# Performance work log

Measured on AMD Instinct MI355X. Metric: run time of the kernel, lower is better.

## Reference

```python
import jax, jax.numpy as jnp
import numpy as np

B, N, PATCH_DIM, HIDDEN, POS_SIZE = 16, 4096, 768, 768, 10240


def setup_inputs() -> dict:
    key = jax.random.key(0)
    k1, k2, k3, k4, k5 = jax.random.split(key, 5)
    pixel_values = jax.random.uniform(k1, (B, N, PATCH_DIM), dtype=jnp.float32)
    pixel_position_ids = jax.random.randint(k2, (B, N, 2), 0, POS_SIZE, dtype=jnp.int32)
    padding_mask = jax.random.randint(k3, (B, N), 0, 2).astype(bool)
    W_proj = jax.random.normal(k4, (HIDDEN, PATCH_DIM), dtype=jnp.float32) * 0.02
    pos_table = jax.random.normal(k5, (2, POS_SIZE, HIDDEN), dtype=jnp.float32) * 0.02
    return {
        "pixel_values": pixel_values,
        "pixel_position_ids": pixel_position_ids,
        "padding_mask": padding_mask,
        "W_proj": W_proj,
        "pos_table": pos_table,
    }


def reference(pixel_values, pixel_position_ids, padding_mask, W_proj, pos_table):
    # Rescale pixels to [-1, 1]
    x = 2.0 * (pixel_values - 0.5)
    # Linear(patch_dim -> hidden), bias=False: h = x @ W^T  -> [B, N, H]
    h = jnp.einsum("bnp,hp->bnh", x, W_proj)
    # Position embedding lookup. Original uses one_hot @ table; mathematically
    # identical to a direct gather per axis followed by a sum over the 2 axes.
    pos = jnp.clip(pixel_position_ids, 0, None)  # [B, N, 2]
    pe = pos_table[0][pos[..., 0]] + pos_table[1][pos[..., 1]]  # [B, N, H]
    pe = jnp.where(padding_mask[..., None], 0.0, pe)
    h = h + pe
    # masked_fill padded positions with 0
    h = jnp.where(padding_mask[..., None], 0.0, h)
    return h
```

## Files before the change

kernel.cpp:

```cpp
#include <hip/hip_runtime.h>
#include <hip/hip_bf16.h>

typedef __bf16 bf16_t;
typedef bf16_t bf16x4 __attribute__((ext_vector_type(4)));
typedef bf16_t bf16x8 __attribute__((ext_vector_type(8)));
typedef float f32x4 __attribute__((ext_vector_type(4)));

constexpr int NB   = 16;
constexpr int NN   = 4096;
constexpr int PD   = 768;
constexpr int HID  = 768;
constexpr int PSZ  = 10240;
constexpr int MT   = NB * NN;
constexpr int BM   = 128;
constexpr int BN   = 128;
constexpr int BK   = 32;
constexpr int NT   = PD / BK;
constexpr int LDSC = 132;
constexpr size_t PVN = (size_t)MT * PD;
constexpr size_t WN  = (size_t)HID * PD;

__device__ __forceinline__ bf16x8 cvt8_affine(const float4& x, const float4& y,
                                              float s, float o) {
    bf16x8 r;
    r[0] = (bf16_t)__builtin_fmaf(s, x.x, o);
    r[1] = (bf16_t)__builtin_fmaf(s, x.y, o);
    r[2] = (bf16_t)__builtin_fmaf(s, x.z, o);
    r[3] = (bf16_t)__builtin_fmaf(s, x.w, o);
    r[4] = (bf16_t)__builtin_fmaf(s, y.x, o);
    r[5] = (bf16_t)__builtin_fmaf(s, y.y, o);
    r[6] = (bf16_t)__builtin_fmaf(s, y.z, o);
    r[7] = (bf16_t)__builtin_fmaf(s, y.w, o);
    return r;
}

__device__ __forceinline__ bf16x4 cvt4_affine(const float4& x, float s, float o) {
    bf16x4 r;
    r[0] = (bf16_t)__builtin_fmaf(s, x.x, o);
    r[1] = (bf16_t)__builtin_fmaf(s, x.y, o);
    r[2] = (bf16_t)__builtin_fmaf(s, x.z, o);
    r[3] = (bf16_t)__builtin_fmaf(s, x.w, o);
    return r;
}

__global__ __launch_bounds__(256)
void compact_cvt(const float* __restrict__ pv,
                 const int* __restrict__ mask,
                 const float* __restrict__ W,
                 bf16_t* __restrict__ Ab,
                 bf16_t* __restrict__ Wb,
                 int* __restrict__ rowmap,
                 int* __restrict__ counter,
                 float* __restrict__ out)
{
    const int bid = blockIdx.x;
    const int tid = threadIdx.x;
    if (bid < 1024) {
        __shared__ int ls_slot[64];
        const int rowbase = bid * 64;
        const int lane = tid & 63;
        const int wv   = tid >> 6;
        if (wv == 0) {
            const int mk = mask[rowbase + lane];
            const unsigned long long b = __ballot(mk == 0);
            const int total = __popcll(b);
            const int pos = __popcll(b & ((1ull << lane) - 1ull));
            int gb = 0;
            if (lane == 0) gb = atomicAdd(counter, total);
            gb = __shfl(gb, 0);
            const int slot = (mk == 0) ? (gb + pos) : -1;
            ls_slot[lane] = slot;
            if (slot >= 0) rowmap[slot] = rowbase + lane;
        }
        __syncthreads();
        for (int i = wv; i < 64; i += 4) {
            const int slot = ls_slot[i];
            const int grow = rowbase + i;
            if (slot >= 0) {
                const float* src = pv + (size_t)grow * PD + lane * 12;
                bf16_t* dst = Ab + (size_t)slot * PD + lane * 12;
                #pragma unroll
                for (int q = 0; q < 3; ++q) {
                    const float4 v = *(const float4*)(src + q * 4);
                    *(bf16x4*)(dst + q * 4) = cvt4_affine(v, 2.f, -1.f);
                }
            } else {
                float* dst = out + (size_t)grow * HID + lane * 12;
                const float4 z{0.f, 0.f, 0.f, 0.f};
                #pragma unroll
                for (int q = 0; q < 3; ++q)
                    *(float4*)(dst + q * 4) = z;
            }
        }
    } else {
        const size_t nu = WN / 8;
        for (size_t u = (size_t)(bid - 1024) * 256 + tid; u < nu;
             u += (size_t)64 * 256) {
            const float4 x = ((const float4*)W)[2 * u];
            const float4 y = ((const float4*)W)[2 * u + 1];
            *(bf16x8*)(Wb + 8 * u) = cvt8_affine(x, y, 1.f, 0.f);
        }
    }
}

__global__ __launch_bounds__(256)
void cvt_kernel(const float* __restrict__ pv, const float* __restrict__ W,
                bf16_t* __restrict__ Ab, bf16_t* __restrict__ Wb)
{
    const size_t nunits = (PVN + WN) / 8;
    const size_t stride = (size_t)gridDim.x * blockDim.x;
    for (size_t u = (size_t)blockIdx.x * blockDim.x + threadIdx.x;
         u < nunits; u += stride) {
        if (u < PVN / 8) {
            const float4 x = ((const float4*)pv)[2 * u];
            const float4 y = ((const float4*)pv)[2 * u + 1];
            *(bf16x8*)(Ab + 8 * u) = cvt8_affine(x, y, 2.f, -1.f);
        } else {
            const size_t v = u - PVN / 8;
            const float4 x = ((const float4*)W)[2 * v];
            const float4 y = ((const float4*)W)[2 * v + 1];
            *(bf16x8*)(Wb + 8 * v) = cvt8_affine(x, y, 1.f, 0.f);
        }
    }
}

__device__ __forceinline__ void gload16(const void* g, void* l) {
    __builtin_amdgcn_global_load_lds(
        (const __attribute__((address_space(1))) void*)g,
        (__attribute__((address_space(3))) void*)l, 16, 0, 0);
}

template <bool USE_MAP>
__global__ __launch_bounds__(256, 4)
void gemm_kernel(const bf16_t* __restrict__ Ab,
                 const bf16_t* __restrict__ Wb,
                 const int* __restrict__ posids,
                 const int* __restrict__ mask,
                 const float* __restrict__ ptab,
                 float* __restrict__ out,
                 const int* __restrict__ rowmap,
                 const int* __restrict__ counter)
{
    __shared__ alignas(16) unsigned char smem[32 * LDSC * 4];
    bf16_t* const Bsb = (bf16_t*)smem;
    float*  const Cs  = (float*)smem;

    int Mc = MT;
    int mt, nt;
    const int bid = blockIdx.x;
    if constexpr (USE_MAP) {
        Mc = counter[0];
        const int Mtiles = (Mc + BM - 1) / BM;
        const int nact = Mtiles * 6;
        if (bid >= nact) return;
        const int q = nact >> 3, rm = nact & 7;
        const int x = bid & 7, i = bid >> 3;
        const int logical = (x < rm ? x * (q + 1) : rm * (q + 1) + (x - rm) * q) + i;
        mt = logical / 6;
        nt = logical - mt * 6;
    } else {
        const int nwg = gridDim.x;
        const int cpx = nwg >> 3;
        const int logical = (bid & 7) * cpx + (bid >> 3);
        mt = logical / 6;
        nt = logical - mt * 6;
    }
    const int row0 = mt * BM;
    const int col0 = nt * BN;

    const int tid  = threadIdx.x;
    const int lane = tid & 63;
    const int wid  = tid >> 6;
    const int wm   = wid >> 1;
    const int wn   = wid & 1;

    const int srow = tid >> 2;
    const int sk   = (tid & 3) * 8;
    const bf16_t* b0 = Wb + (size_t)(col0 + srow) * PD + sk;
    const int lds_lo = srow * BK + sk;
    const int lds_hi = (srow + 64) * BK + sk;

    f32x4 acc[4][4];
    #pragma unroll
    for (int i = 0; i < 4; ++i)
        #pragma unroll
        for (int j = 0; j < 4; ++j)
            acc[i][j] = f32x4{0.f, 0.f, 0.f, 0.f};

    const int lr = lane & 15;
    const int kg = lane >> 4;
    const int b_rd_off = (wn * 64 + lr) * BK + kg * 8;

    const bf16_t* aF[4];
    #pragma unroll
    for (int i = 0; i < 4; ++i)
        aF[i] = Ab + (size_t)(row0 + wm * 64 + i * 16 + lr) * PD + kg * 8;

    gload16(b0,           Bsb + lds_lo);
    gload16(b0 + 64 * PD, Bsb + lds_hi);
    __syncthreads();

    int cur = 0;
    for (int t = 0; t < NT; ++t) {
        bf16x8 af[4];
        #pragma unroll
        for (int i = 0; i < 4; ++i)
            af[i] = *(const bf16x8*)(aF[i] + t * BK);

        if (t + 1 < NT) {
            const int k1 = (t + 1) * BK;
            const int nb = cur ^ 1;
            gload16(b0 + k1,           Bsb + nb * (BN * BK) + lds_lo);
            gload16(b0 + 64 * PD + k1, Bsb + nb * (BN * BK) + lds_hi);
        }

        bf16x8 bfv[4];
        #pragma unroll
        for (int i = 0; i < 4; ++i)
            bfv[i] = *(const bf16x8*)(Bsb + cur * (BN * BK) + b_rd_off + i * 16 * BK);

        #pragma unroll
        for (int i = 0; i < 4; ++i)
            #pragma unroll
            for (int j = 0; j < 4; ++j)
                acc[i][j] = __builtin_amdgcn_mfma_f32_16x16x32_bf16(
                    af[i], bfv[j], acc[i][j], 0, 0, 0);

        __syncthreads();
        cur ^= 1;
    }

    const int lrow_w  = wm * 16 + kg * 4;
    const int lcol_w  = wn * 64 + lr;
    const int rr = tid >> 3;
    const int cg = tid & 7;
    const int erow_local = (rr & 15) + (rr >> 4) * 64;

    int grow4[4], p04[4], p14[4];
    #pragma unroll
    for (int mi = 0; mi < 4; ++mi) {
        int crow = row0 + mi * 16 + erow_local;
        if constexpr (USE_MAP) {
            const int cc = crow < Mc ? crow : Mc - 1;
            grow4[mi] = rowmap[cc];
        } else {
            grow4[mi] = crow;
        }
        int p0 = posids[2 * grow4[mi]];
        int p1 = posids[2 * grow4[mi] + 1];
        p04[mi] = p0 < 0 ? 0 : p0;
        p14[mi] = p1 < 0 ? 0 : p1;
    }

    #pragma unroll
    for (int mi = 0; mi < 4; ++mi) {
        __syncthreads();
        #pragma unroll
        for (int r = 0; r < 4; ++r)
            #pragma unroll
            for (int ni = 0; ni < 4; ++ni)
                Cs[(lrow_w + r) * LDSC + lcol_w + ni * 16] = acc[mi][ni][r];
        __syncthreads();

        const int crow = row0 + mi * 16 + erow_local;
        if constexpr (USE_MAP) {
            if (crow >= Mc) continue;
            const float* t0 = ptab + (size_t)p04[mi] * HID + col0;
            const float* t1 = ptab + (size_t)PSZ * HID + (size_t)p14[mi] * HID + col0;
            float* orow = out + (size_t)grow4[mi] * HID + col0;
            #pragma unroll
            for (int j = 0; j < 4; ++j) {
                const int c = (cg + 8 * j) * 4;
                float4 v  = *(const float4*)&Cs[rr * LDSC + c];
                const float4 e0 = *(const float4*)(t0 + c);
                const float4 e1 = *(const float4*)(t1 + c);
                v.x += e0.x + e1.x;
                v.y += e0.y + e1.y;
                v.z += e0.z + e1.z;
                v.w += e0.w + e1.w;
                *(float4*)(orow + c) = v;
            }
        } else {
            const int grow = crow;
            float* orow = out + (size_t)grow * HID + col0;
            const int mk = mask[grow];
            if (mk) {
                const float4 z{0.f, 0.f, 0.f, 0.f};
                #pragma unroll
                for (int j = 0; j < 4; ++j)
                    *(float4*)(orow + (cg + 8 * j) * 4) = z;
            } else {
                const float* t0 = ptab + (size_t)p04[mi] * HID + col0;
                const float* t1 = ptab + (size_t)PSZ * HID + (size_t)p14[mi] * HID + col0;
                #pragma unroll
                for (int j = 0; j < 4; ++j) {
                    const int c = (cg + 8 * j) * 4;
                    float4 v  = *(const float4*)&Cs[rr * LDSC + c];
                    const float4 e0 = *(const float4*)(t0 + c);
                    const float4 e1 = *(const float4*)(t1 + c);
                    v.x += e0.x + e1.x;
                    v.y += e0.y + e1.y;
                    v.z += e0.z + e1.z;
                    v.w += e0.w + e1.w;
                    *(float4*)(orow + c) = v;
                }
            }
        }
    }
}

constexpr int LDSS = 40;

__global__ __launch_bounds__(256, 2)
void vpe_kernel(const float* __restrict__ pv,
                const int* __restrict__ posids,
                const int* __restrict__ mask,
                const float* __restrict__ W,
                const float* __restrict__ ptab,
                float* __restrict__ out)
{
    __shared__ alignas(16) bf16_t As[2][BM * LDSS];
    __shared__ alignas(16) bf16_t Bs[2][BM * LDSS];

    const int nwg = gridDim.x;
    const int cpx = nwg >> 3;
    const int logical = (blockIdx.x & 7) * cpx + (blockIdx.x >> 3);
    const int mt = logical / 6;
    const int nt = logical - mt * 6;
    const int row0 = mt * BM;
    const int col0 = nt * BN;

    const int tid  = threadIdx.x;
    const int lane = tid & 63;
    const int wid  = tid >> 6;
    const int wm   = wid >> 1;
    const int wn   = wid & 1;
    const int srow = tid >> 1;
    const int scol = (tid & 1) << 4;

    const float* aptr = pv + (size_t)(row0 + srow) * PD + scol;
    const float* bptr = W  + (size_t)(col0 + srow) * PD + scol;
    const int lds_w_off = srow * LDSS + scol;

    f32x4 acc[4][4];
    #pragma unroll
    for (int i = 0; i < 4; ++i)
        #pragma unroll
        for (int j = 0; j < 4; ++j)
            acc[i][j] = f32x4{0.f, 0.f, 0.f, 0.f};

    const int lr = lane & 15;
    const int kg = lane >> 4;
    const int a_rd_off = (wm * 64 + lr) * LDSS + kg * 8;
    const int b_rd_off = (wn * 64 + lr) * LDSS + kg * 8;

    float4 ra[4], rb[4];
    #pragma unroll
    for (int q = 0; q < 4; ++q) {
        ra[q] = *(const float4*)(aptr + q * 4);
        rb[q] = *(const float4*)(bptr + q * 4);
    }
    {
        bf16x8 av0 = cvt8_affine(ra[0], ra[1], 2.f, -1.f);
        bf16x8 av1 = cvt8_affine(ra[2], ra[3], 2.f, -1.f);
        bf16x8 bv0 = cvt8_affine(rb[0], rb[1], 1.f, 0.f);
        bf16x8 bv1 = cvt8_affine(rb[2], rb[3], 1.f, 0.f);
        *(bf16x8*)(&As[0][lds_w_off])     = av0;
        *(bf16x8*)(&As[0][lds_w_off] + 8) = av1;
        *(bf16x8*)(&Bs[0][lds_w_off])     = bv0;
        *(bf16x8*)(&Bs[0][lds_w_off] + 8) = bv1;
    }
    __syncthreads();

    int cur = 0;
    for (int t = 0; t < NT - 1; ++t) {
        const int k1 = (t + 1) * BK;
        #pragma unroll
        for (int q = 0; q < 4; ++q) {
            ra[q] = *(const float4*)(aptr + k1 + q * 4);
            rb[q] = *(const float4*)(bptr + k1 + q * 4);
        }
        bf16x8 af[4], bfv[4];
        #pragma unroll
        for (int i = 0; i < 4; ++i) {
            af[i]  = *(const bf16x8*)(&As[cur][a_rd_off] + i * 16 * LDSS);
            bfv[i] = *(const bf16x8*)(&Bs[cur][b_rd_off] + i * 16 * LDSS);
        }
        #pragma unroll
        for (int i = 0; i < 4; ++i)
            #pragma unroll
            for (int j = 0; j < 4; ++j)
                acc[i][j] = __builtin_amdgcn_mfma_f32_16x16x32_bf16(
                    af[i], bfv[j], acc[i][j], 0, 0, 0);
        {
            bf16x8 av0 = cvt8_affine(ra[0], ra[1], 2.f, -1.f);
            bf16x8 av1 = cvt8_affine(ra[2], ra[3], 2.f, -1.f);
            bf16x8 bv0 = cvt8_affine(rb[0], rb[1], 1.f, 0.f);
            bf16x8 bv1 = cvt8_affine(rb[2], rb[3], 1.f, 0.f);
            const int nb = cur ^ 1;
            *(bf16x8*)(&As[nb][lds_w_off])     = av0;
            *(bf16x8*)(&As[nb][lds_w_off] + 8) = av1;
            *(bf16x8*)(&Bs[nb][lds_w_off])     = bv0;
            *(bf16x8*)(&Bs[nb][lds_w_off] + 8) = bv1;
        }
        __syncthreads();
        cur ^= 1;
    }
    {
        bf16x8 af[4], bfv[4];
        #pragma unroll
        for (int i = 0; i < 4; ++i) {
            af[i]  = *(const bf16x8*)(&As[cur][a_rd_off] + i * 16 * LDSS);
            bfv[i] = *(const bf16x8*)(&Bs[cur][b_rd_off] + i * 16 * LDSS);
        }
        #pragma unroll
        for (int i = 0; i < 4; ++i)
            #pragma unroll
            for (int j = 0; j < 4; ++j)
                acc[i][j] = __builtin_amdgcn_mfma_f32_16x16x32_bf16(
                    af[i], bfv[j], acc[i][j], 0, 0, 0);
    }
    #pragma unroll
    for (int mi = 0; mi < 4; ++mi) {
        #pragma unroll
        for (int r = 0; r < 4; ++r) {
            const int grow = row0 + wm * 64 + mi * 16 + kg * 4 + r;
            const int mk = mask[grow];
            int p0 = posids[2 * grow];
            int p1 = posids[2 * grow + 1];
            p0 = p0 < 0 ? 0 : p0;
            p1 = p1 < 0 ? 0 : p1;
            const float* t0 = ptab + (size_t)p0 * HID;
            const float* t1 = ptab + (size_t)PSZ * HID + (size_t)p1 * HID;
            float* orow = out + (size_t)grow * HID;
            #pragma unroll
            for (int ni = 0; ni < 4; ++ni) {
                const int col = col0 + wn * 64 + ni * 16 + lr;
                const float v = acc[mi][ni][r] + t0[col] + t1[col];
                orow[col] = mk ? 0.f : v;
            }
        }
    }
}

extern "C" void kernel_launch(void* const* d_in, const int* in_sizes, int n_in,
                              void* d_out, int out_size, void* d_ws, size_t ws_size,
                              hipStream_t stream) {
    (void)in_sizes; (void)n_in; (void)out_size;
    const float* pv     = (const float*)d_in[0];
    const int*   posids = (const int*)d_in[1];
    const int*   mask   = (const int*)d_in[2];
    const float* W      = (const float*)d_in[3];
    const float* ptab   = (const float*)d_in[4];
    float*       out    = (float*)d_out;

    const size_t AB_B = PVN * sizeof(bf16_t);
    const size_t WB_B = WN * sizeof(bf16_t);
    const size_t RM_B = (size_t)MT * 4;
    const size_t need1 = AB_B + WB_B;
    const size_t need2 = AB_B + WB_B + RM_B + 16;
    const int grid = (MT / BM) * (HID / BN);

    if (ws_size >= need2) {
        bf16_t* Ab   = (bf16_t*)d_ws;
        bf16_t* Wb   = Ab + PVN;
        int* rowmap  = (int*)((char*)d_ws + AB_B + WB_B);
        int* counter = (int*)((char*)d_ws + AB_B + WB_B + RM_B);
        hipMemsetAsync(counter, 0, 16, stream);
        hipLaunchKernelGGL(compact_cvt, dim3(1088), dim3(256), 0, stream,
                           pv, mask, W, Ab, Wb, rowmap, counter, out);
        hipLaunchKernelGGL((gemm_kernel<true>), dim3(grid), dim3(256), 0, stream,
                           Ab, Wb, posids, mask, ptab, out, rowmap, counter);
    } else if (ws_size >= need1) {
        bf16_t* Ab = (bf16_t*)d_ws;
        bf16_t* Wb = Ab + PVN;
        hipLaunchKernelGGL(cvt_kernel, dim3(2048), dim3(256), 0, stream,
                           pv, W, Ab, Wb);
        hipLaunchKernelGGL((gemm_kernel<false>), dim3(grid), dim3(256), 0, stream,
                           Ab, Wb, posids, mask, ptab, out, nullptr, nullptr);
    } else {
        hipLaunchKernelGGL(vpe_kernel, dim3(grid), dim3(256), 0, stream,
                           pv, posids, mask, W, ptab, out);
    }
}
```

Before: 208.6 us.

## Stage A tiles through LDS with async loads and halve compaction block size

```diff
diff --git a/kernel.cpp b/kernel.cpp
--- a/kernel.cpp
+++ b/kernel.cpp
@@ -55,25 +55,28 @@
 {
     const int bid = blockIdx.x;
     const int tid = threadIdx.x;
-    if (bid < 1024) {
-        __shared__ int ls_slot[64];
-        const int rowbase = bid * 64;
+    if (bid < 2048) {
+        __shared__ int ls_slot[32];
+        const int rowbase = bid * 32;
         const int lane = tid & 63;
         const int wv   = tid >> 6;
         if (wv == 0) {
-            const int mk = mask[rowbase + lane];
+            const bool valid = lane < 32;
+            const int mk = valid ? mask[rowbase + lane] : 1;
             const unsigned long long b = __ballot(mk == 0);
             const int total = __popcll(b);
             const int pos = __popcll(b & ((1ull << lane) - 1ull));
             int gb = 0;
             if (lane == 0) gb = atomicAdd(counter, total);
             gb = __shfl(gb, 0);
-            const int slot = (mk == 0) ? (gb + pos) : -1;
-            ls_slot[lane] = slot;
-            if (slot >= 0) rowmap[slot] = rowbase + lane;
+            if (valid) {
+                const int slot = (mk == 0) ? (gb + pos) : -1;
+                ls_slot[lane] = slot;
+                if (slot >= 0) rowmap[slot] = rowbase + lane;
+            }
         }
         __syncthreads();
-        for (int i = wv; i < 64; i += 4) {
+        for (int i = wv; i < 32; i += 4) {
             const int slot = ls_slot[i];
             const int grow = rowbase + i;
             if (slot >= 0) {
@@ -94,7 +97,7 @@
         }
     } else {
         const size_t nu = WN / 8;
-        for (size_t u = (size_t)(bid - 1024) * 256 + tid; u < nu;
+        for (size_t u = (size_t)(bid - 2048) * 256 + tid; u < nu;
              u += (size_t)64 * 256) {
             const float4 x = ((const float4*)W)[2 * u];
             const float4 y = ((const float4*)W)[2 * u + 1];
@@ -141,8 +144,9 @@
                  const int* __restrict__ rowmap,
                  const int* __restrict__ counter)
 {
-    __shared__ alignas(16) unsigned char smem[32 * LDSC * 4];
-    bf16_t* const Bsb = (bf16_t*)smem;
+    __shared__ alignas(16) unsigned char smem[2 * (BM * BK + BN * BK) * 2];
+    bf16_t* const Asb = (bf16_t*)smem;
+    bf16_t* const Bsb = (bf16_t*)smem + 2 * BM * BK;
     float*  const Cs  = (float*)smem;
 
     int Mc = MT;
@@ -176,6 +180,7 @@
 
     const int srow = tid >> 2;
     const int sk   = (tid & 3) * 8;
+    const bf16_t* a0 = Ab + (size_t)(row0 + srow) * PD + sk;
     const bf16_t* b0 = Wb + (size_t)(col0 + srow) * PD + sk;
     const int lds_lo = srow * BK + sk;
     const int lds_hi = (srow + 64) * BK + sk;
@@ -189,36 +194,32 @@
 
     const int lr = lane & 15;
     const int kg = lane >> 4;
+    const int a_rd_off = (wm * 64 + lr) * BK + kg * 8;
     const int b_rd_off = (wn * 64 + lr) * BK + kg * 8;
 
-    const bf16_t* aF[4];
-    #pragma unroll
-    for (int i = 0; i < 4; ++i)
-        aF[i] = Ab + (size_t)(row0 + wm * 64 + i * 16 + lr) * PD + kg * 8;
-
+    gload16(a0,           Asb + lds_lo);
+    gload16(a0 + 64 * PD, Asb + lds_hi);
     gload16(b0,           Bsb + lds_lo);
     gload16(b0 + 64 * PD, Bsb + lds_hi);
     __syncthreads();
 
     int cur = 0;
     for (int t = 0; t < NT; ++t) {
-        bf16x8 af[4];
-        #pragma unroll
-        for (int i = 0; i < 4; ++i)
-            af[i] = *(const bf16x8*)(aF[i] + t * BK);
-
         if (t + 1 < NT) {
             const int k1 = (t + 1) * BK;
             const int nb = cur ^ 1;
+            gload16(a0 + k1,           Asb + nb * (BM * BK) + lds_lo);
+            gload16(a0 + 64 * PD + k1, Asb + nb * (BM * BK) + lds_hi);
             gload16(b0 + k1,           Bsb + nb * (BN * BK) + lds_lo);
             gload16(b0 + 64 * PD + k1, Bsb + nb * (BN * BK) + lds_hi);
         }
 
-        bf16x8 bfv[4];
-        #pragma unroll
-        for (int i = 0; i < 4; ++i)
+        bf16x8 af[4], bfv[4];
+        #pragma unroll
+        for (int i = 0; i < 4; ++i) {
+            af[i]  = *(const bf16x8*)(Asb + cur * (BM * BK) + a_rd_off + i * 16 * BK);
             bfv[i] = *(const bf16x8*)(Bsb + cur * (BN * BK) + b_rd_off + i * 16 * BK);
-
+        }
         #pragma unroll
         for (int i = 0; i < 4; ++i)
             #pragma unroll
@@ -254,7 +255,7 @@
 
     #pragma unroll
     for (int mi = 0; mi < 4; ++mi) {
-        __syncthreads();
+        if (mi) __syncthreads();
         #pragma unroll
         for (int r = 0; r < 4; ++r)
             #pragma unroll
@@ -467,7 +468,7 @@
         int* rowmap  = (int*)((char*)d_ws + AB_B + WB_B);
         int* counter = (int*)((char*)d_ws + AB_B + WB_B + RM_B);
         hipMemsetAsync(counter, 0, 16, stream);
-        hipLaunchKernelGGL(compact_cvt, dim3(1088), dim3(256), 0, stream,
+        hipLaunchKernelGGL(compact_cvt, dim3(2112), dim3(256), 0, stream,
                            pv, mask, W, Ab, Wb, rowmap, counter, out);
         hipLaunchKernelGGL((gemm_kernel<true>), dim3(grid), dim3(256), 0, stream,
                            Ab, Wb, posids, mask, ptab, out, rowmap, counter);
```

After: 179.4 us. -14.0%, faster.
